# Optimization experiments

Hardware: AMD Instinct MI355X
Metric: run time of the kernel (lower is better)

The kernel has to match this reference:

```python
import jax, jax.numpy as jnp
import numpy as np

B, N, T_IN, F_IN = 16, 30000, 6, 1
E = 120000          # edges per etype
N_ETYPES = 2        # etypes per graph (hg and tg each)
KT, LK = 3, 3
C1, C2 = 8, 11      # block channel sizes
HID = 128


def _conv2d(x, w, b):
    # x: [B,Cin,T,N], w: [Cout,Cin,kt,1] -> valid conv
    y = jax.lax.conv_general_dilated(x, w, window_strides=(1, 1), padding='VALID',
                                     dimension_numbers=('NCHW', 'OIHW', 'NCHW'))
    return y + b[None, :, None, None]


def _glu_tconv(x, w, b, c_out, x_align):
    # TemporalConvLayer with act='GLU'
    xc = _conv2d(x, w, b)
    return (xc[:, :c_out] + x_align) * jax.nn.sigmoid(xc[:, c_out:])


def _hetcheb(X, edges, W, bias):
    # Heterogeneous ChebConv (sum over edge types), lambda_max=2 => L_hat = -D^-1/2 A D^-1/2
    # X: [S,N,Cin], edges: [n_et,2,E] int32, W: [n_et,Lk,Cin,Cout], bias: [n_et,Cout]
    S, n, cin = X.shape
    Lk = W.shape[1]
    Xn = jnp.transpose(X, (1, 0, 2))  # [N,S,Cin]
    out = jnp.zeros((n, S, W.shape[-1]), X.dtype)
    for e in range(edges.shape[0]):
        src, dst = edges[e, 0], edges[e, 1]
        ones = jnp.ones(src.shape, X.dtype)
        deg_in = jnp.clip(jax.ops.segment_sum(ones, dst, num_segments=n), 1.0)
        deg_out = jnp.clip(jax.ops.segment_sum(ones, src, num_segments=n), 1.0)
        norm = jax.lax.rsqrt(deg_out)[src] * jax.lax.rsqrt(deg_in)[dst]  # [E]
        def prop(Tm):  # L_hat @ T = -(Ahat @ T); vectorized over all B*T slices at once
            Tf = Tm.reshape(n, S * cin)
            return -jax.ops.segment_sum(norm[:, None] * Tf[src], dst, num_segments=n).reshape(n, S, cin)
        Tkm2 = Xn
        Tkm1 = prop(Xn)
        z = jnp.einsum('nsc,cd->nsd', Tkm2, W[e, 0]) + jnp.einsum('nsc,cd->nsd', Tkm1, W[e, 1])
        for k in range(2, Lk):
            Tk = 2.0 * prop(Tkm1) - Tkm2
            z = z + jnp.einsum('nsc,cd->nsd', Tk, W[e, k])
            Tkm2, Tkm1 = Tkm1, Tk
        out = out + z + bias[e][None, None, :]
    return jnp.transpose(out, (1, 0, 2))  # [S,N,Cout]


def _block(x, hg_edges, tg_edges, align_fn, tw, tb, hW, hb, tW, tb2, c_out):
    # HetETAConvBlock (dropout = identity in eval)
    x_align = align_fn(x)[:, :, KT - 1:, :]
    x_t1 = _glu_tconv(x, tw, tb, c_out, x_align)          # [B,c_out,T',N]
    b_, c_, t_, n_ = x_t1.shape
    X = jnp.transpose(x_t1, (0, 2, 3, 1)).reshape(b_ * t_, n_, c_)  # batched slices
    xs = _hetcheb(X, hg_edges, hW, hb).reshape(b_, t_, n_, -1).transpose(0, 3, 1, 2)
    xt = _hetcheb(X, tg_edges, tW, tb2).reshape(b_, t_, n_, -1).transpose(0, 3, 1, 2)
    return jnp.concatenate([xs, xt], axis=1)              # [B,2*c_out,T',N]


def setup_inputs() -> dict:
    key = jax.random.key(0)
    ks = jax.random.split(key, 20)
    s = 0.1
    inp = {
        'x': jax.random.normal(ks[0], (B, N, T_IN, F_IN), jnp.float32),
        'hg_edges': jax.random.randint(ks[1], (N_ETYPES, 2, E), 0, N, jnp.int32),
        'tg_edges': jax.random.randint(ks[2], (N_ETYPES, 2, E), 0, N, jnp.int32),
        # block1: tconv GLU 1 -> 8 (out 2*8 channels)
        'tconv1_w': jax.random.normal(ks[3], (2 * C1, F_IN, KT, 1), jnp.float32) * s,
        'tconv1_b': jnp.zeros((2 * C1,), jnp.float32),
        'h1_W': jax.random.normal(ks[4], (N_ETYPES, LK, C1, C1), jnp.float32) * s,
        'h1_b': jnp.zeros((N_ETYPES, C1), jnp.float32),
        't1_W': jax.random.normal(ks[5], (N_ETYPES, LK, C1, C1), jnp.float32) * s,
        't1_b': jnp.zeros((N_ETYPES, C1), jnp.float32),
        # block2: align 16 -> 11 (conv1x1), tconv GLU 16 -> 11
        'align2_w': jax.random.normal(ks[6], (C2, 2 * C1, 1, 1), jnp.float32) * s,
        'align2_b': jnp.zeros((C2,), jnp.float32),
        'tconv2_w': jax.random.normal(ks[7], (2 * C2, 2 * C1, KT, 1), jnp.float32) * s,
        'tconv2_b': jnp.zeros((2 * C2,), jnp.float32),
        'h2_W': jax.random.normal(ks[8], (N_ETYPES, LK, C2, C2), jnp.float32) * s,
        'h2_b': jnp.zeros((N_ETYPES, C2), jnp.float32),
        't2_W': jax.random.normal(ks[9], (N_ETYPES, LK, C2, C2), jnp.float32) * s,
        't2_b': jnp.zeros((N_ETYPES, C2), jnp.float32),
        # output linear: 11*2*(6-2*(3-1)) = 44 -> HID
        'out_w': jax.random.normal(ks[10], (2 * C2 * (T_IN - 2 * (KT - 1)), HID), jnp.float32) * s,
        'out_b': jnp.zeros((HID,), jnp.float32),
    }
    return inp


def reference(x, hg_edges, tg_edges, tconv1_w, tconv1_b, h1_W, h1_b, t1_W, t1_b,
              align2_w, align2_b, tconv2_w, tconv2_b, h2_W, h2_b, t2_W, t2_b,
              out_w, out_b):
    x = jnp.transpose(x, (0, 3, 2, 1))  # [B,1,T,N]
    # block1: Align pads channels 1 -> 8
    align1 = lambda v: jnp.pad(v, ((0, 0), (0, C1 - F_IN), (0, 0), (0, 0)))
    x1 = _block(x, hg_edges, tg_edges, align1, tconv1_w, tconv1_b, h1_W, h1_b, t1_W, t1_b, C1)
    # block2: Align is 1x1 conv 16 -> 11
    align2 = lambda v: _conv2d(v, align2_w, align2_b)
    x2 = _block(x1, hg_edges, tg_edges, align2, tconv2_w, tconv2_b, h2_W, h2_b, t2_W, t2_b, C2)
    b_, c_, t_, n_ = x2.shape
    z = jnp.transpose(x2, (0, 3, 1, 2)).reshape(b_, n_, c_ * t_)  # [B,N,44]
    return z @ out_w + out_b  # [B,N,HID]
```

## Files before the change

kernel.cpp:

```cpp
#include <hip/hip_runtime.h>
#include <hip/hip_fp16.h>
#include <math.h>

#define EDGES 120000
#define NN    30000
#define NCH   118

__device__ __forceinline__ float sigmoidf_(float x) { return 1.f / (1.f + __expf(-x)); }

union F4H8 { float4 v; __half h[8]; };

__device__ __forceinline__ void unpack8(float4 v, float* f) {
  F4H8 u; u.v = v;
#pragma unroll
  for (int i = 0; i < 8; ++i) f[i] = __half2float(u.h[i]);
}
__device__ __forceinline__ float4 pack8(const float* f) {
  F4H8 u;
#pragma unroll
  for (int i = 0; i < 8; ++i) u.h[i] = __float2half(f[i]);
  return u.v;
}
__device__ __forceinline__ void unpack4(float2 v, float* f) {
  union { float2 v; __half h[4]; } u; u.v = v;
#pragma unroll
  for (int i = 0; i < 4; ++i) f[i] = __half2float(u.h[i]);
}

#define CSR_STRIDE 270016
#define CSR_RP(base, l)   ((base) + (size_t)(l) * CSR_STRIDE)
#define CSR_SRC(base, l)  ((base) + (size_t)(l) * CSR_STRIDE + 30016)
#define CSR_NRM(base, l)  ((float*)((base) + (size_t)(l) * CSR_STRIDE + 150016))

__global__ void count_all_kernel(const int* __restrict__ hg, const int* __restrict__ tg,
                                 int* __restrict__ degO, int* __restrict__ degI) {
  int tid = blockIdx.x * blockDim.x + threadIdx.x;
  if (tid >= 4 * EDGES) return;
  int l = tid / EDGES, j = tid - l * EDGES;
  const int* G = (l < 2) ? hg : tg;
  const int* src = G + (size_t)(l & 1) * 2 * EDGES;
  const int* dst = src + EDGES;
  atomicAdd(&degO[l * NN + src[j]], 1);
  atomicAdd(&degI[l * NN + dst[j]], 1);
}

__global__ __launch_bounds__(256) void scan1_kernel(const int* __restrict__ degI,
                                                    int* __restrict__ csrBase,
                                                    int* __restrict__ partials) {
  int l = blockIdx.x / NCH, ch = blockIdx.x - l * NCH;
  int tid = threadIdx.x;
  int i = ch * 256 + tid;
  __shared__ int buf[256];
  int v = (i < NN) ? degI[l * NN + i] : 0;
  buf[tid] = v;
  __syncthreads();
  for (int off = 1; off < 256; off <<= 1) {
    int t = (tid >= off) ? buf[tid - off] : 0;
    __syncthreads();
    buf[tid] += t;
    __syncthreads();
  }
  int* rp = CSR_RP(csrBase, l);
  if (i < NN) rp[i + 1] = buf[tid];
  if (tid == 255) partials[l * NCH + ch] = buf[255];
}

__global__ __launch_bounds__(128) void scan2_kernel(int* __restrict__ partials) {
  __shared__ int buf[128];
  int tid = threadIdx.x;
  for (int l = 0; l < 4; ++l) {
    int v = (tid < NCH) ? partials[l * NCH + tid] : 0;
    buf[tid] = v;
    __syncthreads();
    for (int off = 1; off < 128; off <<= 1) {
      int t = (tid >= off) ? buf[tid - off] : 0;
      __syncthreads();
      buf[tid] += t;
      __syncthreads();
    }
    if (tid < NCH) partials[l * NCH + tid] = buf[tid] - v;
    __syncthreads();
  }
}

__global__ __launch_bounds__(256) void fixup_kernel(int* __restrict__ csrBase,
                                                    int* __restrict__ cursor,
                                                    const int* __restrict__ partials) {
  int l = blockIdx.x / NCH, ch = blockIdx.x - l * NCH;
  int i = ch * 256 + threadIdx.x;
  int* rp = CSR_RP(csrBase, l);
  int off = partials[l * NCH + ch];
  if (i < NN) {
    int val = rp[i + 1] + off;
    rp[i + 1] = val;
    if (i + 1 < NN) cursor[l * NN + i + 1] = val;
  }
  if (i == 0) { rp[0] = 0; cursor[l * NN] = 0; }
}

__global__ void fill_all_kernel(const int* __restrict__ hg, const int* __restrict__ tg,
                                const int* __restrict__ degO, const int* __restrict__ degI,
                                int* __restrict__ cursor, int* __restrict__ csrBase) {
  int tid = blockIdx.x * blockDim.x + threadIdx.x;
  if (tid >= 4 * EDGES) return;
  int l = tid / EDGES, j = tid - l * EDGES;
  const int* G = (l < 2) ? hg : tg;
  const int* src = G + (size_t)(l & 1) * 2 * EDGES;
  const int* dst = src + EDGES;
  int s = src[j], d = dst[j];
  int doo = degO[l * NN + s]; if (doo < 1) doo = 1;
  int dii = degI[l * NN + d]; if (dii < 1) dii = 1;
  float nm = rsqrtf((float)doo) * rsqrtf((float)dii);
  int p = atomicAdd(&cursor[l * NN + d], 1);
  CSR_SRC(csrBase, l)[p] = s;
  CSR_NRM(csrBase, l)[p] = nm;
}

__global__ void glu1_kernel(const float* __restrict__ x, const float* __restrict__ w,
                            const float* __restrict__ b, __half* __restrict__ X1h) {
  int idx = blockIdx.x * blockDim.x + threadIdx.x;
  if (idx >= NN * 64) return;
  int n = idx >> 6, s = idx & 63;
  int bb = s >> 2, t = s & 3;
  const float* xb = x + ((long)bb * NN + n) * 6;
  float x0 = xb[t], x1 = xb[t + 1], x2 = xb[t + 2];
  float o[8];
#pragma unroll
  for (int c = 0; c < 8; ++c) {
    float p = w[c * 3 + 0] * x0 + w[c * 3 + 1] * x1 + w[c * 3 + 2] * x2 + b[c];
    float q = w[(c + 8) * 3 + 0] * x0 + w[(c + 8) * 3 + 1] * x1 + w[(c + 8) * 3 + 2] * x2 + b[c + 8];
    float al = (c == 0) ? x2 : 0.f;
    o[c] = (p + al) * sigmoidf_(q);
  }
  reinterpret_cast<float4*>(X1h)[idx] = pack8(o);
}

__global__ __launch_bounds__(256) void pull_all_kernel(const int* __restrict__ csrBase,
                                                       const __half* __restrict__ Xh,
                                                       __half* __restrict__ T1hAll) {
  int gtid = blockIdx.x * 256 + threadIdx.x;
  int l = gtid / (NN * 64);
  int t = gtid - l * (NN * 64);
  int n = t >> 6, j = t & 63;
  const int* rp = CSR_RP(csrBase, l);
  const int* cs = CSR_SRC(csrBase, l);
  const float* cn = CSR_NRM(csrBase, l);
  const float4* in4 = reinterpret_cast<const float4*>(Xh);
  float acc[8];
#pragma unroll
  for (int i = 0; i < 8; ++i) acc[i] = 0.f;
  int beg = rp[n], end = rp[n + 1];
  for (int e = beg; e < end; ++e) {
    float nm = cn[e];
    float f[8];
    unpack8(in4[(long)cs[e] * 64 + j], f);
#pragma unroll
    for (int i = 0; i < 8; ++i) acc[i] -= nm * f[i];
  }
  reinterpret_cast<float4*>(T1hAll)[gtid] = pack8(acc);
}

__global__ __launch_bounds__(256) void cheb1_kernel(const int* __restrict__ csrBase,
    const __half* __restrict__ Xh, const __half* __restrict__ T1hAll,
    const float* __restrict__ Whg, const float* __restrict__ bhg,
    const float* __restrict__ Wtg, const float* __restrict__ btg,
    __half* __restrict__ outH, __half* __restrict__ outT) {
  constexpr int C = 8, CC = 64;
  __shared__ float wx[CC], w1a[CC], w1b[CC], w2a[CC], w2b[CC], bs[C];
  int gtid = blockIdx.x * 256 + threadIdx.x;
  int g = gtid / (NN * 64);
  int tid = gtid - g * (NN * 64);
  const float* W = g ? Wtg : Whg;
  const float* bias = g ? btg : bhg;
  for (int i = threadIdx.x; i < CC; i += 256) {
    float w0A = W[i], w1A = W[CC + i], w2A = W[2 * CC + i];
    float w0B = W[3 * CC + i], w1B = W[4 * CC + i], w2B = W[5 * CC + i];
    wx[i] = w0A - w2A + w0B - w2B;
    w1a[i] = w1A; w1b[i] = w1B;
    w2a[i] = -2.f * w2A; w2b[i] = -2.f * w2B;
  }
  if (threadIdx.x < C) bs[threadIdx.x] = bias[threadIdx.x] + bias[C + threadIdx.x];
  __syncthreads();
  int n = tid >> 6, s = tid & 63;
  int l0 = 2 * g, l1 = 2 * g + 1;
  const int* rp0 = CSR_RP(csrBase, l0); const int* cs0 = CSR_SRC(csrBase, l0);
  const float* cn0 = CSR_NRM(csrBase, l0);
  const int* rp1 = CSR_RP(csrBase, l1); const int* cs1 = CSR_SRC(csrBase, l1);
  const float* cn1 = CSR_NRM(csrBase, l1);
  const float4* A4 = reinterpret_cast<const float4*>(T1hAll + (size_t)l0 * (NN * 512));
  const float4* B4 = reinterpret_cast<const float4*>(T1hAll + (size_t)l1 * (NN * 512));
  float acc0[C], acc1[C];
#pragma unroll
  for (int c = 0; c < C; ++c) { acc0[c] = 0.f; acc1[c] = 0.f; }
  for (int e = rp0[n], end = rp0[n + 1]; e < end; ++e) {
    float nm = cn0[e];
    float f[8];
    unpack8(A4[(long)cs0[e] * 64 + s], f);
#pragma unroll
    for (int c = 0; c < C; ++c) acc0[c] += nm * f[c];
  }
  for (int e = rp1[n], end = rp1[n + 1]; e < end; ++e) {
    float nm = cn1[e];
    float f[8];
    unpack8(B4[(long)cs1[e] * 64 + s], f);
#pragma unroll
    for (int c = 0; c < C; ++c) acc1[c] += nm * f[c];
  }
  float x0[C], ta[C], tb[C];
  unpack8(reinterpret_cast<const float4*>(Xh)[tid], x0);
  unpack8(A4[tid], ta);
  unpack8(B4[tid], tb);
  float z[C];
#pragma unroll
  for (int d = 0; d < C; ++d) {
    float zz = bs[d];
#pragma unroll
    for (int c = 0; c < C; ++c)
      zz += x0[c] * wx[c * C + d] + ta[c] * w1a[c * C + d] + tb[c] * w1b[c * C + d] +
            acc0[c] * w2a[c * C + d] + acc1[c] * w2b[c * C + d];
    z[d] = zz;
  }
  reinterpret_cast<float4*>(g ? outT : outH)[tid] = pack8(z);
}

__global__ __launch_bounds__(256) void glu2_kernel(const __half* __restrict__ H, const __half* __restrict__ Tt,
                                                   const float* __restrict__ w2, const float* __restrict__ b2,
                                                   const float* __restrict__ aw, const float* __restrict__ ab,
                                                   __half* __restrict__ X2nh) {
  __shared__ float w2s[22 * 16 * 3], b2s[22], aws[11 * 16], abs_[11];
  for (int i = threadIdx.x; i < 22 * 16 * 3; i += 256) w2s[i] = w2[i];
  if (threadIdx.x < 22) b2s[threadIdx.x] = b2[threadIdx.x];
  for (int i = threadIdx.x; i < 11 * 16; i += 256) aws[i] = aw[i];
  if (threadIdx.x < 11) abs_[threadIdx.x] = ab[threadIdx.x];
  __syncthreads();
  int idx = blockIdx.x * 256 + threadIdx.x;
  int n = idx >> 5, s = idx & 31;
  int bb = s >> 1, t = s & 1;
  long rbase = (long)n * 64 + bb * 4 + t;
  const float4* H4 = reinterpret_cast<const float4*>(H) + rbase;
  const float4* T4 = reinterpret_cast<const float4*>(Tt) + rbase;
  float hv[24], tv[24];
  unpack8(H4[0], hv); unpack8(H4[1], hv + 8); unpack8(H4[2], hv + 16);
  unpack8(T4[0], tv); unpack8(T4[1], tv + 8); unpack8(T4[2], tv + 16);
  float o[16];
#pragma unroll
  for (int i = 11; i < 16; ++i) o[i] = 0.f;
#pragma unroll
  for (int co = 0; co < 11; ++co) {
    float p = b2s[co], q = b2s[co + 11], a = abs_[co];
#pragma unroll
    for (int ci = 0; ci < 16; ++ci) {
      float v0 = (ci < 8) ? hv[ci] : tv[ci - 8];
      float v1 = (ci < 8) ? hv[8 + ci] : tv[ci];
      float v2 = (ci < 8) ? hv[16 + ci] : tv[8 + ci];
      p += w2s[(co * 16 + ci) * 3 + 0] * v0 + w2s[(co * 16 + ci) * 3 + 1] * v1 +
           w2s[(co * 16 + ci) * 3 + 2] * v2;
      q += w2s[((co + 11) * 16 + ci) * 3 + 0] * v0 + w2s[((co + 11) * 16 + ci) * 3 + 1] * v1 +
           w2s[((co + 11) * 16 + ci) * 3 + 2] * v2;
      a += aws[co * 16 + ci] * v2;
    }
    o[co] = (p + a) * sigmoidf_(q);
  }
  float4* o4 = reinterpret_cast<float4*>(X2nh) + (long)idx * 2;
  o4[0] = pack8(o);
  o4[1] = pack8(o + 8);
}

__global__ __launch_bounds__(256) void cheb2_kernel(const int* __restrict__ csrBase,
    const __half* __restrict__ Xh, const __half* __restrict__ T1hAll,
    const float* __restrict__ Whg, const float* __restrict__ bhg,
    const float* __restrict__ Wtg, const float* __restrict__ btg,
    float* __restrict__ outH, float* __restrict__ outT) {
  constexpr int C = 11, CC = 121;
  __shared__ float wx[CC], w1a[CC], w1b[CC], w2a[CC], w2b[CC], bs[C];
  int gtid = blockIdx.x * 256 + threadIdx.x;
  int g = gtid / (NN * 32);
  int tid = gtid - g * (NN * 32);
  const float* W = g ? Wtg : Whg;
  const float* bias = g ? btg : bhg;
  for (int i = threadIdx.x; i < CC; i += 256) {
    float w0A = W[i], w1A = W[CC + i], w2A = W[2 * CC + i];
    float w0B = W[3 * CC + i], w1B = W[4 * CC + i], w2B = W[5 * CC + i];
    wx[i] = w0A - w2A + w0B - w2B;
    w1a[i] = w1A; w1b[i] = w1B;
    w2a[i] = -2.f * w2A; w2b[i] = -2.f * w2B;
  }
  if (threadIdx.x < C) bs[threadIdx.x] = bias[threadIdx.x] + bias[C + threadIdx.x];
  __syncthreads();
  int n = tid >> 5, s = tid & 31;
  int l0 = 2 * g, l1 = 2 * g + 1;
  const int* rp0 = CSR_RP(csrBase, l0); const int* cs0 = CSR_SRC(csrBase, l0);
  const float* cn0 = CSR_NRM(csrBase, l0);
  const int* rp1 = CSR_RP(csrBase, l1); const int* cs1 = CSR_SRC(csrBase, l1);
  const float* cn1 = CSR_NRM(csrBase, l1);
  const __half* T1a = T1hAll + (size_t)l0 * (NN * 512);
  const __half* T1b = T1hAll + (size_t)l1 * (NN * 512);
  const float4* A4 = reinterpret_cast<const float4*>(T1a);
  const float2* A2 = reinterpret_cast<const float2*>(T1a);
  const float4* B4 = reinterpret_cast<const float4*>(T1b);
  const float2* B2 = reinterpret_cast<const float2*>(T1b);
  float acc0[12], acc1[12];
#pragma unroll
  for (int c = 0; c < 12; ++c) { acc0[c] = 0.f; acc1[c] = 0.f; }
  for (int e = rp0[n], end = rp0[n + 1]; e < end; ++e) {
    float nm = cn0[e];
    long src = cs0[e];
    float f[12];
    unpack8(A4[src * 64 + s * 2], f);
    unpack4(A2[src * 128 + s * 4 + 2], f + 8);
#pragma unroll
    for (int c = 0; c < 12; ++c) acc0[c] += nm * f[c];
  }
  for (int e = rp1[n], end = rp1[n + 1]; e < end; ++e) {
    float nm = cn1[e];
    long src = cs1[e];
    float f[12];
    unpack8(B4[src * 64 + s * 2], f);
    unpack4(B2[src * 128 + s * 4 + 2], f + 8);
#pragma unroll
    for (int c = 0; c < 12; ++c) acc1[c] += nm * f[c];
  }
  float x0[12], ta[12], tb[12];
  {
    const float4* X4 = reinterpret_cast<const float4*>(Xh);
    const float2* X2 = reinterpret_cast<const float2*>(Xh);
    unpack8(X4[(long)tid * 2], x0);     unpack4(X2[(long)tid * 4 + 2], x0 + 8);
    unpack8(A4[(long)tid * 2], ta);     unpack4(A2[(long)tid * 4 + 2], ta + 8);
    unpack8(B4[(long)tid * 2], tb);     unpack4(B2[(long)tid * 4 + 2], tb + 8);
  }
  float z[12];
#pragma unroll
  for (int d = 0; d < C; ++d) {
    float zz = bs[d];
#pragma unroll
    for (int c = 0; c < C; ++c)
      zz += x0[c] * wx[c * C + d] + ta[c] * w1a[c * C + d] + tb[c] * w1b[c * C + d] +
            acc0[c] * w2a[c * C + d] + acc1[c] * w2b[c * C + d];
    z[d] = zz;
  }
  z[11] = 0.f;
  float4* o4 = reinterpret_cast<float4*>(g ? outT : outH) + (long)tid * 3;
  o4[0] = make_float4(z[0], z[1], z[2], z[3]);
  o4[1] = make_float4(z[4], z[5], z[6], z[7]);
  o4[2] = make_float4(z[8], z[9], z[10], 0.f);
}

__global__ __launch_bounds__(256) void final_kernel(const float* __restrict__ H2, const float* __restrict__ T2b,
                                                    const float* __restrict__ W, const float* __restrict__ bias,
                                                    float* __restrict__ out) {
  __shared__ float zsr[64][48];
  int tid = threadIdx.x;
  long r0 = (long)blockIdx.x * 64;
#pragma unroll
  for (int it = 0; it < 3; ++it) {
    int item = it * 256 + tid;
    int row = item / 12, piece = item - row * 12;
    long r = r0 + row;
    int b = (int)(r / NN), n = (int)(r - (long)b * NN);
    const float4* srcb = reinterpret_cast<const float4*>(piece < 6 ? H2 : T2b);
    int f4i = (piece < 6) ? piece : piece - 6;
    float4 v = srcb[((long)n * 32 + b * 2) * 3 + f4i];
    *reinterpret_cast<float4*>(&zsr[row][(piece < 6 ? 0 : 24) + f4i * 4]) = v;
  }
  int c = tid & 127, h = tid >> 7;
  float wp[48];
#pragma unroll
  for (int off = 0; off < 48; ++off) {
    int half_ = off / 24, r_ = off - half_ * 24;
    int t = r_ / 12, c_ = r_ - t * 12;
    wp[off] = (c_ == 11) ? 0.f : W[(2 * (c_ + half_ * 11) + t) * 128 + c];
  }
  float bh = bias[c];
  __syncthreads();
  int rbeg = h * 32;
#pragma unroll 2
  for (int row = rbeg; row < rbeg + 32; ++row) {
    const float4* zr4 = reinterpret_cast<const float4*>(&zsr[row][0]);
    float acc = bh;
#pragma unroll
    for (int q = 0; q < 12; ++q) {
      float4 zv = zr4[q];
      acc = fmaf(zv.x, wp[4 * q + 0], acc);
      acc = fmaf(zv.y, wp[4 * q + 1], acc);
      acc = fmaf(zv.z, wp[4 * q + 2], acc);
      acc = fmaf(zv.w, wp[4 * q + 3], acc);
    }
    out[(r0 + row) * 128 + c] = acc;
  }
}

extern "C" void kernel_launch(void* const* d_in, const int* in_sizes, int n_in,
                              void* d_out, int out_size, void* d_ws, size_t ws_size,
                              hipStream_t stream) {
  const float* x    = (const float*)d_in[0];
  const int*   hg   = (const int*)d_in[1];
  const int*   tg   = (const int*)d_in[2];
  const float* t1w  = (const float*)d_in[3];
  const float* t1b  = (const float*)d_in[4];
  const float* h1W  = (const float*)d_in[5];
  const float* h1b  = (const float*)d_in[6];
  const float* g1W  = (const float*)d_in[7];
  const float* g1b  = (const float*)d_in[8];
  const float* a2w  = (const float*)d_in[9];
  const float* a2b  = (const float*)d_in[10];
  const float* t2w  = (const float*)d_in[11];
  const float* t2b  = (const float*)d_in[12];
  const float* h2W  = (const float*)d_in[13];
  const float* h2b  = (const float*)d_in[14];
  const float* g2W  = (const float*)d_in[15];
  const float* g2b  = (const float*)d_in[16];
  const float* outw = (const float*)d_in[17];
  const float* outb = (const float*)d_in[18];
  float* out = (float*)d_out;

  __half* T1h = (__half*)d_ws;
  __half* X1h = T1h + 4u * 15360000;
  __half* Cfh = X1h + 15360000;
  __half* Dfh = Cfh + 15360000;
  float*  Cf  = (float*)(Dfh + 15360000);
  float*  Df  = Cf + 11520000;
  int* csrBase  = (int*)(Df + 11520000);
  int* degO     = (int*)Cf;
  int* degI     = degO + 4 * NN;
  int* cursor   = degI + 4 * NN;
  int* partials = cursor + 4 * NN;

  hipMemsetAsync(degO, 0, 8 * NN * sizeof(int), stream);
  count_all_kernel<<<(4 * EDGES + 255) / 256, 256, 0, stream>>>(hg, tg, degO, degI);
  scan1_kernel<<<4 * NCH, 256, 0, stream>>>(degI, csrBase, partials);
  scan2_kernel<<<1, 128, 0, stream>>>(partials);
  fixup_kernel<<<4 * NCH, 256, 0, stream>>>(csrBase, cursor, partials);
  fill_all_kernel<<<(4 * EDGES + 255) / 256, 256, 0, stream>>>(hg, tg, degO, degI, cursor, csrBase);

  glu1_kernel<<<NN * 64 / 256, 256, 0, stream>>>(x, t1w, t1b, X1h);
  pull_all_kernel<<<4 * NN * 64 / 256, 256, 0, stream>>>(csrBase, X1h, T1h);
  cheb1_kernel<<<2 * NN * 64 / 256, 256, 0, stream>>>(csrBase, X1h, T1h, h1W, h1b, g1W, g1b, Cfh, Dfh);

  glu2_kernel<<<NN * 32 / 256, 256, 0, stream>>>(Cfh, Dfh, t2w, t2b, a2w, a2b, X1h);
  pull_all_kernel<<<4 * NN * 64 / 256, 256, 0, stream>>>(csrBase, X1h, T1h);
  cheb2_kernel<<<2 * NN * 32 / 256, 256, 0, stream>>>(csrBase, X1h, T1h, h2W, h2b, g2W, g2b, Cf, Df);

  final_kernel<<<7500, 256, 0, stream>>>(Cf, Df, outw, outb, out);
}
```

Baseline: 891.8 us.

## Pack CSR src/norm pairs, shrink block-2 features to 12-channel fp16, unroll gathers

Interleaves each CSR entry's source index and norm into one int2, so a single load fetches both. Block-2 activations shrink from 16 padded half channels to 12, via a new pull2 kernel, and the cheb2 outputs become fp16 instead of fp32. Final_kernel now reads half data. The gather loops are unrolled by 4 in the pull kernels and by 2 in cheb to keep more loads in flight. The aim is to cut bytes moved in the memory-bound sparse gathers, at the cost of extra fp16 rounding on the block-2 outputs.

```diff
diff --git a/kernel.cpp b/kernel.cpp
--- a/kernel.cpp
+++ b/kernel.cpp
@@ -5,10 +5,12 @@
 #define EDGES 120000
 #define NN    30000
 #define NCH   118
+#define T1SLOT 15360000
 
 __device__ __forceinline__ float sigmoidf_(float x) { return 1.f / (1.f + __expf(-x)); }
 
 union F4H8 { float4 v; __half h[8]; };
+union F2H4 { float2 v; __half h[4]; };
 
 __device__ __forceinline__ void unpack8(float4 v, float* f) {
   F4H8 u; u.v = v;
@@ -22,15 +24,21 @@
   return u.v;
 }
 __device__ __forceinline__ void unpack4(float2 v, float* f) {
-  union { float2 v; __half h[4]; } u; u.v = v;
+  F2H4 u; u.v = v;
 #pragma unroll
   for (int i = 0; i < 4; ++i) f[i] = __half2float(u.h[i]);
+}
+__device__ __forceinline__ float2 pack4(const float* f) {
+  F2H4 u;
+#pragma unroll
+  for (int i = 0; i < 4; ++i) u.h[i] = __float2half(f[i]);
+  return u.v;
 }
 
 #define CSR_STRIDE 270016
 #define CSR_RP(base, l)   ((base) + (size_t)(l) * CSR_STRIDE)
-#define CSR_SRC(base, l)  ((base) + (size_t)(l) * CSR_STRIDE + 30016)
-#define CSR_NRM(base, l)  ((float*)((base) + (size_t)(l) * CSR_STRIDE + 150016))
+#define CSR_PK(base, l)   ((const int2*)((base) + (size_t)(l) * CSR_STRIDE + 30016))
+#define CSR_PKW(base, l)  ((int2*)((base) + (size_t)(l) * CSR_STRIDE + 30016))
 
 __global__ void count_all_kernel(const int* __restrict__ hg, const int* __restrict__ tg,
                                  int* __restrict__ degO, int* __restrict__ degI) {
@@ -112,8 +120,7 @@
   int dii = degI[l * NN + d]; if (dii < 1) dii = 1;
   float nm = rsqrtf((float)doo) * rsqrtf((float)dii);
   int p = atomicAdd(&cursor[l * NN + d], 1);
-  CSR_SRC(csrBase, l)[p] = s;
-  CSR_NRM(csrBase, l)[p] = nm;
+  CSR_PKW(csrBase, l)[p] = make_int2(s, __float_as_int(nm));
 }
 
 __global__ void glu1_kernel(const float* __restrict__ x, const float* __restrict__ w,
@@ -135,29 +142,52 @@
   reinterpret_cast<float4*>(X1h)[idx] = pack8(o);
 }
 
-__global__ __launch_bounds__(256) void pull_all_kernel(const int* __restrict__ csrBase,
-                                                       const __half* __restrict__ Xh,
-                                                       __half* __restrict__ T1hAll) {
+__global__ __launch_bounds__(256) void pull1_kernel(const int* __restrict__ csrBase,
+                                                    const __half* __restrict__ Xh,
+                                                    __half* __restrict__ T1hAll) {
   int gtid = blockIdx.x * 256 + threadIdx.x;
   int l = gtid / (NN * 64);
   int t = gtid - l * (NN * 64);
   int n = t >> 6, j = t & 63;
   const int* rp = CSR_RP(csrBase, l);
-  const int* cs = CSR_SRC(csrBase, l);
-  const float* cn = CSR_NRM(csrBase, l);
+  const int2* pk = CSR_PK(csrBase, l);
   const float4* in4 = reinterpret_cast<const float4*>(Xh);
   float acc[8];
 #pragma unroll
   for (int i = 0; i < 8; ++i) acc[i] = 0.f;
-  int beg = rp[n], end = rp[n + 1];
-  for (int e = beg; e < end; ++e) {
-    float nm = cn[e];
+  int e = rp[n], end = rp[n + 1];
+  for (; e + 4 <= end; e += 4) {
+    int2 p0 = pk[e], p1 = pk[e + 1], p2 = pk[e + 2], p3 = pk[e + 3];
+    float4 v0 = in4[(long)p0.x * 64 + j];
+    float4 v1 = in4[(long)p1.x * 64 + j];
+    float4 v2 = in4[(long)p2.x * 64 + j];
+    float4 v3 = in4[(long)p3.x * 64 + j];
     float f[8];
-    unpack8(in4[(long)cs[e] * 64 + j], f);
+    float n0 = __int_as_float(p0.y), n1 = __int_as_float(p1.y);
+    float n2 = __int_as_float(p2.y), n3 = __int_as_float(p3.y);
+    unpack8(v0, f);
+#pragma unroll
+    for (int i = 0; i < 8; ++i) acc[i] -= n0 * f[i];
+    unpack8(v1, f);
+#pragma unroll
+    for (int i = 0; i < 8; ++i) acc[i] -= n1 * f[i];
+    unpack8(v2, f);
+#pragma unroll
+    for (int i = 0; i < 8; ++i) acc[i] -= n2 * f[i];
+    unpack8(v3, f);
+#pragma unroll
+    for (int i = 0; i < 8; ++i) acc[i] -= n3 * f[i];
+  }
+  for (; e < end; ++e) {
+    int2 p = pk[e];
+    float4 v = in4[(long)p.x * 64 + j];
+    float nm = __int_as_float(p.y);
+    float f[8];
+    unpack8(v, f);
 #pragma unroll
     for (int i = 0; i < 8; ++i) acc[i] -= nm * f[i];
   }
-  reinterpret_cast<float4*>(T1hAll)[gtid] = pack8(acc);
+  reinterpret_cast<float4*>(T1hAll)[(size_t)l * (T1SLOT / 8) + t] = pack8(acc);
 }
 
 __global__ __launch_bounds__(256) void cheb1_kernel(const int* __restrict__ csrBase,
@@ -183,42 +213,71 @@
   __syncthreads();
   int n = tid >> 6, s = tid & 63;
   int l0 = 2 * g, l1 = 2 * g + 1;
-  const int* rp0 = CSR_RP(csrBase, l0); const int* cs0 = CSR_SRC(csrBase, l0);
-  const float* cn0 = CSR_NRM(csrBase, l0);
-  const int* rp1 = CSR_RP(csrBase, l1); const int* cs1 = CSR_SRC(csrBase, l1);
-  const float* cn1 = CSR_NRM(csrBase, l1);
-  const float4* A4 = reinterpret_cast<const float4*>(T1hAll + (size_t)l0 * (NN * 512));
-  const float4* B4 = reinterpret_cast<const float4*>(T1hAll + (size_t)l1 * (NN * 512));
+  const int* rp0 = CSR_RP(csrBase, l0); const int2* pk0 = CSR_PK(csrBase, l0);
+  const int* rp1 = CSR_RP(csrBase, l1); const int2* pk1 = CSR_PK(csrBase, l1);
+  const float4* A4 = reinterpret_cast<const float4*>(T1hAll + (size_t)l0 * T1SLOT);
+  const float4* B4 = reinterpret_cast<const float4*>(T1hAll + (size_t)l1 * T1SLOT);
   float acc0[C], acc1[C];
 #pragma unroll
   for (int c = 0; c < C; ++c) { acc0[c] = 0.f; acc1[c] = 0.f; }
-  for (int e = rp0[n], end = rp0[n + 1]; e < end; ++e) {
-    float nm = cn0[e];
-    float f[8];
-    unpack8(A4[(long)cs0[e] * 64 + s], f);
-#pragma unroll
-    for (int c = 0; c < C; ++c) acc0[c] += nm * f[c];
-  }
-  for (int e = rp1[n], end = rp1[n + 1]; e < end; ++e) {
-    float nm = cn1[e];
-    float f[8];
-    unpack8(B4[(long)cs1[e] * 64 + s], f);
-#pragma unroll
-    for (int c = 0; c < C; ++c) acc1[c] += nm * f[c];
-  }
-  float x0[C], ta[C], tb[C];
-  unpack8(reinterpret_cast<const float4*>(Xh)[tid], x0);
-  unpack8(A4[tid], ta);
-  unpack8(B4[tid], tb);
+  {
+    int e = rp0[n], end = rp0[n + 1];
+    for (; e + 2 <= end; e += 2) {
+      int2 p0 = pk0[e], p1 = pk0[e + 1];
+      float4 v0 = A4[(long)p0.x * 64 + s];
+      float4 v1 = A4[(long)p1.x * 64 + s];
+      float n0 = __int_as_float(p0.y), n1 = __int_as_float(p1.y);
+      float f0[8], f1[8];
+      unpack8(v0, f0); unpack8(v1, f1);
+#pragma unroll
+      for (int c = 0; c < C; ++c) acc0[c] += n0 * f0[c] + n1 * f1[c];
+    }
+    for (; e < end; ++e) {
+      int2 p = pk0[e];
+      float4 v = A4[(long)p.x * 64 + s];
+      float nm = __int_as_float(p.y);
+      float f[8]; unpack8(v, f);
+#pragma unroll
+      for (int c = 0; c < C; ++c) acc0[c] += nm * f[c];
+    }
+  }
+  {
+    int e = rp1[n], end = rp1[n + 1];
+    for (; e + 2 <= end; e += 2) {
+      int2 p0 = pk1[e], p1 = pk1[e + 1];
+      float4 v0 = B4[(long)p0.x * 64 + s];
+      float4 v1 = B4[(long)p1.x * 64 + s];
+      float n0 = __int_as_float(p0.y), n1 = __int_as_float(p1.y);
+      float f0[8], f1[8];
+      unpack8(v0, f0); unpack8(v1, f1);
+#pragma unroll
+      for (int c = 0; c < C; ++c) acc1[c] += n0 * f0[c] + n1 * f1[c];
+    }
+    for (; e < end; ++e) {
+      int2 p = pk1[e];
+      float4 v = B4[(long)p.x * 64 + s];
+      float nm = __int_as_float(p.y);
+      float f[8]; unpack8(v, f);
+#pragma unroll
+      for (int c = 0; c < C; ++c) acc1[c] += nm * f[c];
+    }
+  }
   float z[C];
 #pragma unroll
-  for (int d = 0; d < C; ++d) {
-    float zz = bs[d];
-#pragma unroll
-    for (int c = 0; c < C; ++c)
-      zz += x0[c] * wx[c * C + d] + ta[c] * w1a[c * C + d] + tb[c] * w1b[c * C + d] +
-            acc0[c] * w2a[c * C + d] + acc1[c] * w2b[c * C + d];
-    z[d] = zz;
+  for (int d = 0; d < C; ++d) z[d] = bs[d];
+  {
+    float xv[8], av[8], bv[8];
+    unpack8(reinterpret_cast<const float4*>(Xh)[tid], xv);
+    unpack8(A4[tid], av);
+    unpack8(B4[tid], bv);
+#pragma unroll
+    for (int c = 0; c < C; ++c) {
+      float x0c = xv[c], tac = av[c], tbc = bv[c], a0 = acc0[c], a1 = acc1[c];
+#pragma unroll
+      for (int d = 0; d < C; ++d)
+        z[d] += x0c * wx[c * C + d] + tac * w1a[c * C + d] + tbc * w1b[c * C + d] +
+                a0 * w2a[c * C + d] + a1 * w2b[c * C + d];
+    }
   }
   reinterpret_cast<float4*>(g ? outT : outH)[tid] = pack8(z);
 }
@@ -242,9 +301,8 @@
   float hv[24], tv[24];
   unpack8(H4[0], hv); unpack8(H4[1], hv + 8); unpack8(H4[2], hv + 16);
   unpack8(T4[0], tv); unpack8(T4[1], tv + 8); unpack8(T4[2], tv + 16);
-  float o[16];
-#pragma unroll
-  for (int i = 11; i < 16; ++i) o[i] = 0.f;
+  float o[12];
+  o[11] = 0.f;
 #pragma unroll
   for (int co = 0; co < 11; ++co) {
     float p = b2s[co], q = b2s[co + 11], a = abs_[co];
@@ -261,16 +319,65 @@
     }
     o[co] = (p + a) * sigmoidf_(q);
   }
-  float4* o4 = reinterpret_cast<float4*>(X2nh) + (long)idx * 2;
-  o4[0] = pack8(o);
-  o4[1] = pack8(o + 8);
+  float2* o2 = reinterpret_cast<float2*>(X2nh) + (long)idx * 3;
+  o2[0] = pack4(o);
+  o2[1] = pack4(o + 4);
+  o2[2] = pack4(o + 8);
+}
+
+__global__ __launch_bounds__(256) void pull2_kernel(const int* __restrict__ csrBase,
+                                                    const __half* __restrict__ Xh,
+                                                    __half* __restrict__ T1hAll) {
+  int gtid = blockIdx.x * 256 + threadIdx.x;
+  int l = gtid / (NN * 96);
+  int t = gtid - l * (NN * 96);
+  int n = t / 96, j = t - n * 96;
+  const int* rp = CSR_RP(csrBase, l);
+  const int2* pk = CSR_PK(csrBase, l);
+  const float2* in2 = reinterpret_cast<const float2*>(Xh);
+  float acc[4];
+#pragma unroll
+  for (int i = 0; i < 4; ++i) acc[i] = 0.f;
+  int e = rp[n], end = rp[n + 1];
+  for (; e + 4 <= end; e += 4) {
+    int2 p0 = pk[e], p1 = pk[e + 1], p2 = pk[e + 2], p3 = pk[e + 3];
+    float2 v0 = in2[(long)p0.x * 96 + j];
+    float2 v1 = in2[(long)p1.x * 96 + j];
+    float2 v2 = in2[(long)p2.x * 96 + j];
+    float2 v3 = in2[(long)p3.x * 96 + j];
+    float f[4];
+    float n0 = __int_as_float(p0.y), n1 = __int_as_float(p1.y);
+    float n2 = __int_as_float(p2.y), n3 = __int_as_float(p3.y);
+    unpack4(v0, f);
+#pragma unroll
+    for (int i = 0; i < 4; ++i) acc[i] -= n0 * f[i];
+    unpack4(v1, f);
+#pragma unroll
+    for (int i = 0; i < 4; ++i) acc[i] -= n1 * f[i];
+    unpack4(v2, f);
+#pragma unroll
+    for (int i = 0; i < 4; ++i) acc[i] -= n2 * f[i];
+    unpack4(v3, f);
+#pragma unroll
+    for (int i = 0; i < 4; ++i) acc[i] -= n3 * f[i];
+  }
+  for (; e < end; ++e) {
+    int2 p = pk[e];
+    float2 v = in2[(long)p.x * 96 + j];
+    float nm = __int_as_float(p.y);
+    float f[4];
+    unpack4(v, f);
+#pragma unroll
+    for (int i = 0; i < 4; ++i) acc[i] -= nm * f[i];
+  }
+  reinterpret_cast<float2*>(T1hAll)[(size_t)l * (T1SLOT / 4) + t] = pack4(acc);
 }
 
 __global__ __launch_bounds__(256) void cheb2_kernel(const int* __restrict__ csrBase,
     const __half* __restrict__ Xh, const __half* __restrict__ T1hAll,
     const float* __restrict__ Whg, const float* __restrict__ bhg,
     const float* __restrict__ Wtg, const float* __restrict__ btg,
-    float* __restrict__ outH, float* __restrict__ outT) {
+    __half* __restrict__ outH, __half* __restrict__ outT) {
   constexpr int C = 11, CC = 121;
   __shared__ float wx[CC], w1a[CC], w1b[CC], w2a[CC], w2b[CC], bs[C];
   int gtid = blockIdx.x * 256 + threadIdx.x;
@@ -288,79 +395,152 @@
   if (threadIdx.x < C) bs[threadIdx.x] = bias[threadIdx.x] + bias[C + threadIdx.x];
   __syncthreads();
   int n = tid >> 5, s = tid & 31;
+  int s3 = s * 3;
   int l0 = 2 * g, l1 = 2 * g + 1;
-  const int* rp0 = CSR_RP(csrBase, l0); const int* cs0 = CSR_SRC(csrBase, l0);
-  const float* cn0 = CSR_NRM(csrBase, l0);
-  const int* rp1 = CSR_RP(csrBase, l1); const int* cs1 = CSR_SRC(csrBase, l1);
-  const float* cn1 = CSR_NRM(csrBase, l1);
-  const __half* T1a = T1hAll + (size_t)l0 * (NN * 512);
-  const __half* T1b = T1hAll + (size_t)l1 * (NN * 512);
-  const float4* A4 = reinterpret_cast<const float4*>(T1a);
-  const float2* A2 = reinterpret_cast<const float2*>(T1a);
-  const float4* B4 = reinterpret_cast<const float4*>(T1b);
-  const float2* B2 = reinterpret_cast<const float2*>(T1b);
+  const int* rp0 = CSR_RP(csrBase, l0); const int2* pk0 = CSR_PK(csrBase, l0);
+  const int* rp1 = CSR_RP(csrBase, l1); const int2* pk1 = CSR_PK(csrBase, l1);
+  const float2* A2v = reinterpret_cast<const float2*>(T1hAll + (size_t)l0 * T1SLOT);
+  const float2* B2v = reinterpret_cast<const float2*>(T1hAll + (size_t)l1 * T1SLOT);
   float acc0[12], acc1[12];
 #pragma unroll
   for (int c = 0; c < 12; ++c) { acc0[c] = 0.f; acc1[c] = 0.f; }
-  for (int e = rp0[n], end = rp0[n + 1]; e < end; ++e) {
-    float nm = cn0[e];
-    long src = cs0[e];
-    float f[12];
-    unpack8(A4[src * 64 + s * 2], f);
-    unpack4(A2[src * 128 + s * 4 + 2], f + 8);
-#pragma unroll
-    for (int c = 0; c < 12; ++c) acc0[c] += nm * f[c];
-  }
-  for (int e = rp1[n], end = rp1[n + 1]; e < end; ++e) {
-    float nm = cn1[e];
-    long src = cs1[e];
-    float f[12];
-    unpack8(B4[src * 64 + s * 2], f);
-    unpack4(B2[src * 128 + s * 4 + 2], f + 8);
-#pragma unroll
-    for (int c = 0; c < 12; ++c) acc1[c] += nm * f[c];
-  }
-  float x0[12], ta[12], tb[12];
   {
-    const float4* X4 = reinterpret_cast<const float4*>(Xh);
-    const float2* X2 = reinterpret_cast<const float2*>(Xh);
-    unpack8(X4[(long)tid * 2], x0);     unpack4(X2[(long)tid * 4 + 2], x0 + 8);
-    unpack8(A4[(long)tid * 2], ta);     unpack4(A2[(long)tid * 4 + 2], ta + 8);
-    unpack8(B4[(long)tid * 2], tb);     unpack4(B2[(long)tid * 4 + 2], tb + 8);
+    int e = rp0[n], end = rp0[n + 1];
+    for (; e + 2 <= end; e += 2) {
+      int2 p0 = pk0[e], p1 = pk0[e + 1];
+      long r0 = (long)p0.x * 96 + s3, r1 = (long)p1.x * 96 + s3;
+      float2 a0 = A2v[r0], a1 = A2v[r0 + 1], a2 = A2v[r0 + 2];
+      float2 b0 = A2v[r1], b1 = A2v[r1 + 1], b2 = A2v[r1 + 2];
+      float n0 = __int_as_float(p0.y), n1 = __int_as_float(p1.y);
+      float f[4];
+      unpack4(a0, f);
+#pragma unroll
+      for (int i = 0; i < 4; ++i) acc0[i] += n0 * f[i];
+      unpack4(a1, f);
+#pragma unroll
+      for (int i = 0; i < 4; ++i) acc0[4 + i] += n0 * f[i];
+      unpack4(a2, f);
+#pragma unroll
+      for (int i = 0; i < 4; ++i) acc0[8 + i] += n0 * f[i];
+      unpack4(b0, f);
+#pragma unroll
+      for (int i = 0; i < 4; ++i) acc0[i] += n1 * f[i];
+      unpack4(b1, f);
+#pragma unroll
+      for (int i = 0; i < 4; ++i) acc0[4 + i] += n1 * f[i];
+      unpack4(b2, f);
+#pragma unroll
+      for (int i = 0; i < 4; ++i) acc0[8 + i] += n1 * f[i];
+    }
+    for (; e < end; ++e) {
+      int2 p = pk0[e];
+      long r = (long)p.x * 96 + s3;
+      float2 a0 = A2v[r], a1 = A2v[r + 1], a2 = A2v[r + 2];
+      float nm = __int_as_float(p.y);
+      float f[4];
+      unpack4(a0, f);
+#pragma unroll
+      for (int i = 0; i < 4; ++i) acc0[i] += nm * f[i];
+      unpack4(a1, f);
+#pragma unroll
+      for (int i = 0; i < 4; ++i) acc0[4 + i] += nm * f[i];
+      unpack4(a2, f);
+#pragma unroll
+      for (int i = 0; i < 4; ++i) acc0[8 + i] += nm * f[i];
+    }
+  }
+  {
+    int e = rp1[n], end = rp1[n + 1];
+    for (; e + 2 <= end; e += 2) {
+      int2 p0 = pk1[e], p1 = pk1[e + 1];
+      long r0 = (long)p0.x * 96 + s3, r1 = (long)p1.x * 96 + s3;
+      float2 a0 = B2v[r0], a1 = B2v[r0 + 1], a2 = B2v[r0 + 2];
+      float2 b0 = B2v[r1], b1 = B2v[r1 + 1], b2 = B2v[r1 + 2];
+      float n0 = __int_as_float(p0.y), n1 = __int_as_float(p1.y);
+      float f[4];
+      unpack4(a0, f);
+#pragma unroll
+      for (int i = 0; i < 4; ++i) acc1[i] += n0 * f[i];
+      unpack4(a1, f);
+#pragma unroll
+      for (int i = 0; i < 4; ++i) acc1[4 + i] += n0 * f[i];
+      unpack4(a2, f);
+#pragma unroll
+      for (int i = 0; i < 4; ++i) acc1[8 + i] += n0 * f[i];
+      unpack4(b0, f);
+#pragma unroll
+      for (int i = 0; i < 4; ++i) acc1[i] += n1 * f[i];
+      unpack4(b1, f);
+#pragma unroll
+      for (int i = 0; i < 4; ++i) acc1[4 + i] += n1 * f[i];
+      unpack4(b2, f);
+#pragma unroll
+      for (int i = 0; i < 4; ++i) acc1[8 + i] += n1 * f[i];
+    }
+    for (; e < end; ++e) {
+      int2 p = pk1[e];
+      long r = (long)p.x * 96 + s3;
+      float2 a0 = B2v[r], a1 = B2v[r + 1], a2 = B2v[r + 2];
+      float nm = __int_as_float(p.y);
+      float f[4];
+      unpack4(a0, f);
+#pragma unroll
+      for (int i = 0; i < 4; ++i) acc1[i] += nm * f[i];
+      unpack4(a1, f);
+#pragma unroll
+      for (int i = 0; i < 4; ++i) acc1[4 + i] += nm * f[i];
+      unpack4(a2, f);
+#pragma unroll
+      for (int i = 0; i < 4; ++i) acc1[8 + i] += nm * f[i];
+    }
   }
   float z[12];
 #pragma unroll
-  for (int d = 0; d < C; ++d) {
-    float zz = bs[d];
-#pragma unroll
-    for (int c = 0; c < C; ++c)
-      zz += x0[c] * wx[c * C + d] + ta[c] * w1a[c * C + d] + tb[c] * w1b[c * C + d] +
-            acc0[c] * w2a[c * C + d] + acc1[c] * w2b[c * C + d];
-    z[d] = zz;
-  }
+  for (int d = 0; d < C; ++d) z[d] = bs[d];
   z[11] = 0.f;
-  float4* o4 = reinterpret_cast<float4*>(g ? outT : outH) + (long)tid * 3;
-  o4[0] = make_float4(z[0], z[1], z[2], z[3]);
-  o4[1] = make_float4(z[4], z[5], z[6], z[7]);
-  o4[2] = make_float4(z[8], z[9], z[10], 0.f);
-}
-
-__global__ __launch_bounds__(256) void final_kernel(const float* __restrict__ H2, const float* __restrict__ T2b,
+  const float2* X2v = reinterpret_cast<const float2*>(Xh);
+  long own = (long)tid * 3;
+#pragma unroll
+  for (int q = 0; q < 3; ++q) {
+    float xv[4], av[4], bv[4];
+    unpack4(X2v[own + q], xv);
+    unpack4(A2v[own + q], av);
+    unpack4(B2v[own + q], bv);
+#pragma unroll
+    for (int k = 0; k < 4; ++k) {
+      int c = q * 4 + k;
+      if (c == 11) continue;
+      float x0c = xv[k], tac = av[k], tbc = bv[k], a0 = acc0[c], a1 = acc1[c];
+#pragma unroll
+      for (int d = 0; d < C; ++d)
+        z[d] += x0c * wx[c * C + d] + tac * w1a[c * C + d] + tbc * w1b[c * C + d] +
+                a0 * w2a[c * C + d] + a1 * w2b[c * C + d];
+    }
+  }
+  float2* o2 = reinterpret_cast<float2*>(g ? outT : outH) + (long)tid * 3;
+  o2[0] = pack4(z);
+  o2[1] = pack4(z + 4);
+  o2[2] = pack4(z + 8);
+}
+
+__global__ __launch_bounds__(256) void final_kernel(const __half* __restrict__ H2, const __half* __restrict__ T2b,
                                                     const float* __restrict__ W, const float* __restrict__ bias,
                                                     float* __restrict__ out) {
-  __shared__ float zsr[64][48];
+  __shared__ __half zsr[64][48];
   int tid = threadIdx.x;
   long r0 = (long)blockIdx.x * 64;
 #pragma unroll
-  for (int it = 0; it < 3; ++it) {
+  for (int it = 0; it < 2; ++it) {
     int item = it * 256 + tid;
-    int row = item / 12, piece = item - row * 12;
-    long r = r0 + row;
-    int b = (int)(r / NN), n = (int)(r - (long)b * NN);
-    const float4* srcb = reinterpret_cast<const float4*>(piece < 6 ? H2 : T2b);
-    int f4i = (piece < 6) ? piece : piece - 6;
-    float4 v = srcb[((long)n * 32 + b * 2) * 3 + f4i];
-    *reinterpret_cast<float4*>(&zsr[row][(piece < 6 ? 0 : 24) + f4i * 4]) = v;
+    if (item < 384) {
+      int row = item / 6, piece = item - row * 6;
+      long r = r0 + row;
+      int b = (int)(r / NN), n = (int)(r - (long)b * NN);
+      const float4* srcb = reinterpret_cast<const float4*>(piece < 3 ? H2 : T2b);
+      int f4i = (piece < 3) ? piece : piece - 3;
+      float4 v = srcb[(long)n * 48 + b * 3 + f4i];
+      *reinterpret_cast<float4*>(&zsr[row][(piece < 3 ? 0 : 24) + f4i * 8]) = v;
+    }
   }
   int c = tid & 127, h = tid >> 7;
   float wp[48];
@@ -378,12 +558,11 @@
     const float4* zr4 = reinterpret_cast<const float4*>(&zsr[row][0]);
     float acc = bh;
 #pragma unroll
-    for (int q = 0; q < 12; ++q) {
-      float4 zv = zr4[q];
-      acc = fmaf(zv.x, wp[4 * q + 0], acc);
-      acc = fmaf(zv.y, wp[4 * q + 1], acc);
-      acc = fmaf(zv.z, wp[4 * q + 2], acc);
-      acc = fmaf(zv.w, wp[4 * q + 3], acc);
+    for (int q = 0; q < 6; ++q) {
+      F4H8 u; u.v = zr4[q];
+#pragma unroll
+      for (int i = 0; i < 8; ++i)
+        acc = fmaf(__half2float(u.h[i]), wp[q * 8 + i], acc);
     }
     out[(r0 + row) * 128 + c] = acc;
   }
@@ -414,13 +593,11 @@
   float* out = (float*)d_out;
 
   __half* T1h = (__half*)d_ws;
-  __half* X1h = T1h + 4u * 15360000;
-  __half* Cfh = X1h + 15360000;
-  __half* Dfh = Cfh + 15360000;
-  float*  Cf  = (float*)(Dfh + 15360000);
-  float*  Df  = Cf + 11520000;
-  int* csrBase  = (int*)(Df + 11520000);
-  int* degO     = (int*)Cf;
+  __half* Xh  = T1h + 4L * T1SLOT;
+  __half* Cfh = Xh + T1SLOT;
+  __half* Dfh = Cfh + T1SLOT;
+  int* csrBase  = (int*)(Dfh + T1SLOT);
+  int* degO     = csrBase + 4 * CSR_STRIDE;
   int* degI     = degO + 4 * NN;
   int* cursor   = degI + 4 * NN;
   int* partials = cursor + 4 * NN;
@@ -432,13 +609,13 @@
   fixup_kernel<<<4 * NCH, 256, 0, stream>>>(csrBase, cursor, partials);
   fill_all_kernel<<<(4 * EDGES + 255) / 256, 256, 0, stream>>>(hg, tg, degO, degI, cursor, csrBase);
 
-  glu1_kernel<<<NN * 64 / 256, 256, 0, stream>>>(x, t1w, t1b, X1h);
-  pull_all_kernel<<<4 * NN * 64 / 256, 256, 0, stream>>>(csrBase, X1h, T1h);
-  cheb1_kernel<<<2 * NN * 64 / 256, 256, 0, stream>>>(csrBase, X1h, T1h, h1W, h1b, g1W, g1b, Cfh, Dfh);
-
-  glu2_kernel<<<NN * 32 / 256, 256, 0, stream>>>(Cfh, Dfh, t2w, t2b, a2w, a2b, X1h);
-  pull_all_kernel<<<4 * NN * 64 / 256, 256, 0, stream>>>(csrBase, X1h, T1h);
-  cheb2_kernel<<<2 * NN * 32 / 256, 256, 0, stream>>>(csrBase, X1h, T1h, h2W, h2b, g2W, g2b, Cf, Df);
-
-  final_kernel<<<7500, 256, 0, stream>>>(Cf, Df, outw, outb, out);
-}
+  glu1_kernel<<<NN * 64 / 256, 256, 0, stream>>>(x, t1w, t1b, Xh);
+  pull1_kernel<<<4 * NN * 64 / 256, 256, 0, stream>>>(csrBase, Xh, T1h);
+  cheb1_kernel<<<2 * NN * 64 / 256, 256, 0, stream>>>(csrBase, Xh, T1h, h1W, h1b, g1W, g1b, Cfh, Dfh);
+
+  glu2_kernel<<<NN * 32 / 256, 256, 0, stream>>>(Cfh, Dfh, t2w, t2b, a2w, a2b, Xh);
+  pull2_kernel<<<4 * NN * 96 / 256, 256, 0, stream>>>(csrBase, Xh, T1h);
+  cheb2_kernel<<<2 * NN * 32 / 256, 256, 0, stream>>>(csrBase, Xh, T1h, h2W, h2b, g2W, g2b, Cfh, Dfh);
+
+  final_kernel<<<7500, 256, 0, stream>>>(Cfh, Dfh, outw, outb, out);
+}
```

New measurement: 831.1 us. -6.8%, faster.
